# Kernel optimization log

Measured on AMD Instinct MI355X. Metric: run time of the kernel, lower is better.

The kernel has to match this reference:

```python
import jax, jax.numpy as jnp
import numpy as np

THRESHOLD = 0.7
STRIDE = 1
PADDING = 1


def setup_inputs() -> dict:
    key = jax.random.key(0)
    k1, k2 = jax.random.split(key)
    B, CIN, H, W = 32, 256, 56, 56
    COUT, K = 256, 3
    x = jax.random.normal(k1, (B, CIN, H, W), dtype=jnp.float32)
    # kaiming-uniform-ish init: U(-bound, bound), bound = sqrt(6/fan_in)
    fan_in = CIN * K * K
    bound = float(np.sqrt(6.0 / fan_in))
    weight = jax.random.uniform(k2, (COUT, CIN, K, K), dtype=jnp.float32,
                                minval=-bound, maxval=bound)
    alpha = jnp.ones((1,), dtype=jnp.float32)
    bias = jnp.zeros((COUT,), dtype=jnp.float32)
    return {"x": x, "weight": weight, "alpha": alpha, "bias": bias}


def _ternize_ste(w, threshold):
    delta = threshold * jnp.mean(jnp.abs(jax.lax.stop_gradient(w)))
    ternary = jnp.where(w > delta, 1.0,
                        jnp.where(w < -delta, -1.0, 0.0)).astype(w.dtype)
    # straight-through: value = ternary, gradient = identity w.r.t. w
    return ternary + (w - jax.lax.stop_gradient(w))


def reference(x, weight, alpha, bias):
    w_t = _ternize_ste(weight, THRESHOLD) * alpha  # [COUT, CIN, K, K]
    out = jax.lax.conv_general_dilated(
        x, w_t,
        window_strides=(STRIDE, STRIDE),
        padding=[(PADDING, PADDING), (PADDING, PADDING)],
        dimension_numbers=("NCHW", "OIHW", "NCHW"),
    )
    return out + bias[None, :, None, None]
```

## Files before the change

kernel.cpp:

```cpp
#include <hip/hip_runtime.h>

typedef unsigned short ushort_t;
typedef short short8 __attribute__((ext_vector_type(8)));
typedef unsigned short ushort8 __attribute__((ext_vector_type(8)));
typedef float floatx4 __attribute__((ext_vector_type(4)));

#define N_W 589824

static __device__ __forceinline__ unsigned short f2bf(float f) {
    unsigned int u = __float_as_uint(f);
    u = (u + 0x7FFFu + ((u >> 16) & 1u)) >> 16;
    return (unsigned short)u;
}

static __device__ __forceinline__ void g2l16(const void* g, void* lds_base_uniform) {
    __builtin_amdgcn_global_load_lds(
        (__attribute__((address_space(1))) void*)g,
        (__attribute__((address_space(3))) void*)lds_base_uniform,
        16, 0, 0);
}

__global__ void absmean_kernel(const float* __restrict__ w, double* __restrict__ dsum) {
    int tid = blockIdx.x * blockDim.x + threadIdx.x;
    int stride = gridDim.x * blockDim.x;
    float local = 0.f;
    for (int i = tid; i < N_W; i += stride) local += fabsf(w[i]);
    for (int off = 32; off > 0; off >>= 1)
        local += __shfl_down(local, off, 64);
    __shared__ float part[4];
    int lane = threadIdx.x & 63, wv = threadIdx.x >> 6;
    if (lane == 0) part[wv] = local;
    __syncthreads();
    if (threadIdx.x == 0) {
        float s = part[0] + part[1] + part[2] + part[3];
        atomicAdd(dsum, (double)s);
    }
}

__global__ void ternarize_frag_kernel(const float* __restrict__ w, const double* __restrict__ dsum,
                                      ushort_t* __restrict__ wtf) {
    int o = blockIdx.x * 256 + threadIdx.x;
    float delta = 0.7f * (float)(*dsum / (double)N_W);
    int e   = o & 7;
    int l   = (o >> 3) & 15;
    int q   = (o >> 7) & 3;
    int i   = (o >> 9) & 3;
    int g   = (o >> 11) & 3;
    int t13 = o >> 13;
    int r9  = t13 % 9;
    int cb  = t13 / 9;
    int co  = g * 64 + i * 16 + l;
    int cin = cb * 32 + q * 8 + e;
    float v = w[(co * 256 + cin) * 9 + r9];
    float t = (v > delta) ? 1.f : ((v < -delta) ? -1.f : 0.f);
    wtf[o] = f2bf(t);
}

__global__ void ternarize_kernel(const float* __restrict__ w, const double* __restrict__ dsum,
                                 ushort_t* __restrict__ wt) {
    int o = blockIdx.x * 256 + threadIdx.x;
    float delta = 0.7f * (float)(*dsum / (double)N_W);
    int cin = o & 255;
    int co  = (o >> 8) & 255;
    int r   = o >> 16;
    float v = w[(co * 256 + cin) * 9 + r];
    float t = (v > delta) ? 1.f : ((v < -delta) ? -1.f : 0.f);
    wt[o] = f2bf(t);
}

__global__ void border_zero_kernel(ushort_t* __restrict__ xp) {
    int e = blockIdx.x * 256 + threadIdx.x;
    int cg   = e & 31;
    int rest = e >> 5;
    int pid  = rest % 228;
    int b    = rest / 228;
    int hh, ww;
    if (pid < 58)       { hh = 0;  ww = pid; }
    else if (pid < 116) { hh = 57; ww = pid - 58; }
    else {
        int p = pid - 116;
        hh = 1 + (p >> 1);
        ww = (p & 1) ? 57 : 0;
    }
    ushort8 z = (ushort8){0,0,0,0,0,0,0,0};
    *(ushort8*)&xp[(((b * 58 + hh) * 58 + ww) << 8) + cg * 8] = z;
}

__global__ __launch_bounds__(256)
void xcvt_kernel(const float* __restrict__ x, ushort_t* __restrict__ xp) {
    __shared__ float tile[64][65];
    const int px0 = blockIdx.x * 64;
    const int ci0 = blockIdx.y * 64;
    const int b   = blockIdx.z;
    const int row  = threadIdx.x >> 6;
    const int lane = threadIdx.x & 63;
#pragma unroll
    for (int k = 0; k < 16; ++k) {
        int ci_l = row * 16 + k;
        tile[ci_l][lane] = x[(b * 256 + ci0 + ci_l) * 3136 + px0 + lane];
    }
    __syncthreads();
#pragma unroll
    for (int p = 0; p < 2; ++p) {
        int c    = threadIdx.x + p * 256;
        int px_l = c >> 3;
        int cg   = c & 7;
        int px = px0 + px_l;
        int h = px / 56, w = px - h * 56;
        ushort8 v;
#pragma unroll
        for (int j = 0; j < 8; ++j) v[j] = f2bf(tile[cg * 8 + j][px_l]);
        *(ushort8*)&xp[(((b * 58 + h + 1) * 58 + (w + 1)) << 8) + ci0 + cg * 8] = v;
    }
}

__global__ __launch_bounds__(256, 3)
void conv_mfma3_kernel(const ushort_t* __restrict__ xp, const ushort_t* __restrict__ wtf,
                       const float* __restrict__ alpha, const float* __restrict__ bias,
                       float* __restrict__ out) {
    __shared__ __align__(16) ushort_t lds_x[2 * 768 * 8];

    const int tid  = threadIdx.x;
    const int b    = blockIdx.y;
    const int th   = blockIdx.x >> 2;
    const int tw   = blockIdx.x & 3;
    const int h0   = th * 8;
    const int w0   = tw * 16;
    const int co0  = blockIdx.z * 128;

    const int lane = tid & 63;
    const int wave = tid >> 6;
    const int l15  = lane & 15;
    const int quad = lane >> 4;
    const int wco  = (wave & 1) * 64;
    const int wrow = (wave >> 1) * 4;

    unsigned goff[3], loff[3];
#pragma unroll
    for (int t = 0; t < 3; ++t) {
        int s = tid + t * 256;
        int ss = (s < 720) ? s : 719;
        int hr = ss / 72;
        int rem = ss - hr * 72;
        int hc = rem >> 2, cig = rem & 3;
        int gh = h0 + hr;
        int gw = w0 + hc; if (gw > 57) gw = 57;
        goff[t] = (unsigned)(((((b * 58 + gh) * 58 + gw) << 8) + (cig << 3)) * 2);
        loff[t] = (unsigned)((s & ~63) * 16);
    }
    const char* xpb = (const char*)xp;

    floatx4 acc[4][4];
#pragma unroll
    for (int i = 0; i < 4; ++i)
#pragma unroll
        for (int j = 0; j < 4; ++j)
            acc[i][j] = (floatx4){0.f, 0.f, 0.f, 0.f};

    const int gsel = blockIdx.z * 2 + (wave & 1);
    const ushort_t* wbase = wtf + gsel * 2048 + lane * 8;

#pragma unroll
    for (int t = 0; t < 3; ++t)
        g2l16(xpb + goff[t], (char*)lds_x + loff[t]);

    int cur = 0;
    for (int cb = 0; cb < 8; ++cb) {
        const ushort_t* wcb = wbase + cb * (9 * 4 * 2048);
        short8 af[3][4];
#pragma unroll
        for (int r = 0; r < 3; ++r)
#pragma unroll
            for (int i = 0; i < 4; ++i)
                af[r][i] = *(const short8*)(wcb + r * 8192 + i * 512);

        __syncthreads();

        if (cb < 7) {
#pragma unroll
            for (int t = 0; t < 3; ++t)
                g2l16(xpb + goff[t] + (cb + 1) * 64, (char*)lds_x + loff[t] + (cur ^ 1) * 12288);
        }

        const ushort_t* xb = lds_x + cur * 6144;

        short8 bfv[2][4];
#pragma unroll
        for (int j = 0; j < 4; ++j)
            bfv[0][j] = *(const short8*)&xb[((wrow + j + 0) * 18 + (l15 + 0)) * 32 + quad * 8];

#pragma unroll
        for (int r9 = 0; r9 < 9; ++r9) {
            if (r9 < 8) {
                const int kh1 = (r9 + 1) / 3;
                const int kw1 = (r9 + 1) - kh1 * 3;
#pragma unroll
                for (int j = 0; j < 4; ++j)
                    bfv[(r9 + 1) & 1][j] = *(const short8*)&xb[((wrow + j + kh1) * 18 + (l15 + kw1)) * 32 + quad * 8];
            }
#pragma unroll
            for (int i = 0; i < 4; ++i)
#pragma unroll
                for (int j = 0; j < 4; ++j)
                    acc[i][j] = __builtin_amdgcn_mfma_f32_16x16x32_bf16(af[r9 % 3][i], bfv[r9 & 1][j], acc[i][j], 0, 0, 0);
            if (r9 < 6) {
#pragma unroll
                for (int i = 0; i < 4; ++i)
                    af[r9 % 3][i] = *(const short8*)(wcb + (r9 + 3) * 8192 + i * 512);
            }
        }
        cur ^= 1;
    }

    const float a0 = alpha[0];
#pragma unroll
    for (int i = 0; i < 4; ++i) {
        int cob = co0 + wco + i * 16 + quad * 4;
#pragma unroll
        for (int j = 0; j < 4; ++j) {
            int hh = h0 + wrow + j;
            int ww = w0 + l15;
            if (ww < 56) {
#pragma unroll
                for (int r = 0; r < 4; ++r) {
                    int cog = cob + r;
                    out[((b * 256 + cog) * 56 + hh) * 56 + ww] = acc[i][j][r] * a0 + bias[cog];
                }
            }
        }
    }
}

__global__ __launch_bounds__(256, 2)
void conv_mfma_fallback_kernel(const float* __restrict__ x, const ushort_t* __restrict__ wt,
                               const float* __restrict__ alpha, const float* __restrict__ bias,
                               float* __restrict__ out) {
    __shared__ __align__(16) ushort_t lds_x[10 * 18 * 40];
    __shared__ __align__(16) ushort_t lds_a[128 * 40];
    const int tid  = threadIdx.x;
    const int b    = blockIdx.y;
    const int th   = blockIdx.x >> 2;
    const int tw   = blockIdx.x & 3;
    const int h0   = th * 8;
    const int w0   = tw * 16;
    const int co0  = blockIdx.z * 128;
    const int lane = tid & 63;
    const int wave = tid >> 6;
    const int l15  = lane & 15;
    const int quad = lane >> 4;
    const int wco  = (wave & 1) * 64;
    const int wrow = (wave >> 1) * 4;
    floatx4 acc[4][4];
#pragma unroll
    for (int i = 0; i < 4; ++i)
#pragma unroll
        for (int j = 0; j < 4; ++j)
            acc[i][j] = (floatx4){0.f, 0.f, 0.f, 0.f};
    const int co_l = tid >> 1;
    const int half = tid & 1;
    for (int cin0 = 0; cin0 < 256; cin0 += 32) {
        for (int e = tid; e < 5760; e += 256) {
            int hc = e % 18;
            int t2 = e / 18;
            int hr = t2 % 10;
            int ci = t2 / 10;
            int hh = h0 - 1 + hr;
            int ww = w0 - 1 + hc;
            float v = 0.f;
            if (hh >= 0 && hh < 56 && ww >= 0 && ww < 56)
                v = x[((b * 256 + cin0 + ci) * 3136) + hh * 56 + ww];
            lds_x[(hr * 18 + hc) * 40 + ci] = f2bf(v);
        }
        for (int r9 = 0; r9 < 9; ++r9) {
            {
                const short8* src = (const short8*)(wt + (((r9 * 256) + co0 + co_l) * 256 + cin0 + half * 16));
                short8 v0 = src[0];
                short8 v1 = src[1];
                *(short8*)&lds_a[co_l * 40 + half * 16]     = v0;
                *(short8*)&lds_a[co_l * 40 + half * 16 + 8] = v1;
            }
            __syncthreads();
            const int kh = r9 / 3;
            const int kw = r9 % 3;
            short8 af[4], bf[4];
#pragma unroll
            for (int j = 0; j < 4; ++j)
                bf[j] = *(const short8*)&lds_x[((wrow + j + kh) * 18 + (l15 + kw)) * 40 + quad * 8];
#pragma unroll
            for (int i = 0; i < 4; ++i)
                af[i] = *(const short8*)&lds_a[(wco + i * 16 + l15) * 40 + quad * 8];
#pragma unroll
            for (int i = 0; i < 4; ++i)
#pragma unroll
                for (int j = 0; j < 4; ++j)
                    acc[i][j] = __builtin_amdgcn_mfma_f32_16x16x32_bf16(af[i], bf[j], acc[i][j], 0, 0, 0);
            __syncthreads();
        }
    }
    const float a0 = alpha[0];
#pragma unroll
    for (int i = 0; i < 4; ++i) {
        int cob = co0 + wco + i * 16 + quad * 4;
#pragma unroll
        for (int j = 0; j < 4; ++j) {
            int hh = h0 + wrow + j;
            int ww = w0 + l15;
            if (ww < 56) {
#pragma unroll
                for (int r = 0; r < 4; ++r) {
                    int cog = cob + r;
                    out[((b * 256 + cog) * 56 + hh) * 56 + ww] = acc[i][j][r] * a0 + bias[cog];
                }
            }
        }
    }
}

extern "C" void kernel_launch(void* const* d_in, const int* in_sizes, int n_in,
                              void* d_out, int out_size, void* d_ws, size_t ws_size,
                              hipStream_t stream) {
    const float* x      = (const float*)d_in[0];
    const float* weight = (const float*)d_in[1];
    const float* alpha  = (const float*)d_in[2];
    const float* bias   = (const float*)d_in[3];
    float* out = (float*)d_out;

    double*   dsum = (double*)d_ws;
    ushort_t* wtf  = (ushort_t*)((char*)d_ws + 256);
    ushort_t* xp   = (ushort_t*)((char*)d_ws + 256 + 1179648);
    const size_t NEED = 256 + 1179648 + 55115776;

    hipMemsetAsync(d_ws, 0, 16, stream);
    absmean_kernel<<<256, 256, 0, stream>>>(weight, dsum);

    dim3 grid(28, 32, 2);
    if (ws_size >= NEED) {
        ternarize_frag_kernel<<<N_W / 256, 256, 0, stream>>>(weight, dsum, wtf);
        border_zero_kernel<<<912, 256, 0, stream>>>(xp);
        dim3 cgrid(49, 4, 32);
        xcvt_kernel<<<cgrid, 256, 0, stream>>>(x, xp);
        conv_mfma3_kernel<<<grid, 256, 0, stream>>>(xp, wtf, alpha, bias, out);
    } else {
        ternarize_kernel<<<N_W / 256, 256, 0, stream>>>(weight, dsum, wtf);
        conv_mfma_fallback_kernel<<<grid, 256, 0, stream>>>(x, wtf, alpha, bias, out);
    }
}
```

Measured before the change: 366.7 us.

## Retile conv to 8x8 pixels by all 256 output channels per block

The main conv kernel now gives each block an 8x8 pixel tile and all 256 output channels, with each wave owning 64 channels. Before, a block covered 8x16 pixels (with masked padding columns) and 128 channels. The aim is to drop the wasted padded columns, reuse each input halo across every output channel, and shrink the LDS footprint. Weight fragments for the next channel block are prefetched during the last taps, and s_setprio raises priority around the MFMA bursts. The cost is that each block now loads more weight data relative to the smaller activation tile, and the halo overhead grows.

```diff
diff --git a/kernel.cpp b/kernel.cpp
--- a/kernel.cpp
+++ b/kernel.cpp
@@ -115,36 +115,35 @@
 }
 
 __global__ __launch_bounds__(256, 3)
-void conv_mfma3_kernel(const ushort_t* __restrict__ xp, const ushort_t* __restrict__ wtf,
+void conv_mfma4_kernel(const ushort_t* __restrict__ xp, const ushort_t* __restrict__ wtf,
                        const float* __restrict__ alpha, const float* __restrict__ bias,
                        float* __restrict__ out) {
-    __shared__ __align__(16) ushort_t lds_x[2 * 768 * 8];
+    __shared__ __align__(16) ushort_t lds_x[2 * 512 * 8];
 
     const int tid  = threadIdx.x;
     const int b    = blockIdx.y;
-    const int th   = blockIdx.x >> 2;
-    const int tw   = blockIdx.x & 3;
+    const int th   = blockIdx.x / 7;
+    const int tw   = blockIdx.x - th * 7;
     const int h0   = th * 8;
-    const int w0   = tw * 16;
-    const int co0  = blockIdx.z * 128;
+    const int w0   = tw * 8;
 
     const int lane = tid & 63;
     const int wave = tid >> 6;
     const int l15  = lane & 15;
     const int quad = lane >> 4;
-    const int wco  = (wave & 1) * 64;
-    const int wrow = (wave >> 1) * 4;
-
-    unsigned goff[3], loff[3];
-#pragma unroll
-    for (int t = 0; t < 3; ++t) {
-        int s = tid + t * 256;
-        int ss = (s < 720) ? s : 719;
-        int hr = ss / 72;
-        int rem = ss - hr * 72;
-        int hc = rem >> 2, cig = rem & 3;
+    const int hs   = l15 >> 3;
+    const int ws   = l15 & 7;
+
+    unsigned goff[2], loff[2];
+#pragma unroll
+    for (int t = 0; t < 2; ++t) {
+        int s  = tid + t * 256;
+        int ss = (s < 400) ? s : 399;
+        int hr  = ss / 40;
+        int rem = ss - hr * 40;
+        int wc  = rem >> 2, cig = rem & 3;
         int gh = h0 + hr;
-        int gw = w0 + hc; if (gw > 57) gw = 57;
+        int gw = w0 + wc;
         goff[t] = (unsigned)(((((b * 58 + gh) * 58 + gw) << 8) + (cig << 3)) * 2);
         loff[t] = (unsigned)((s & ~63) * 16);
     }
@@ -157,37 +156,41 @@
         for (int j = 0; j < 4; ++j)
             acc[i][j] = (floatx4){0.f, 0.f, 0.f, 0.f};
 
-    const int gsel = blockIdx.z * 2 + (wave & 1);
+    const int gsel = wave;
     const ushort_t* wbase = wtf + gsel * 2048 + lane * 8;
 
-#pragma unroll
-    for (int t = 0; t < 3; ++t)
+    short8 af[3][4];
+#pragma unroll
+    for (int r = 0; r < 3; ++r)
+#pragma unroll
+        for (int i = 0; i < 4; ++i)
+            af[r][i] = *(const short8*)(wbase + r * 8192 + i * 512);
+
+#pragma unroll
+    for (int t = 0; t < 2; ++t)
         g2l16(xpb + goff[t], (char*)lds_x + loff[t]);
+
+    const int baseB = (hs * 10 + ws) * 32 + quad * 8;
 
     int cur = 0;
     for (int cb = 0; cb < 8; ++cb) {
-        const ushort_t* wcb = wbase + cb * (9 * 4 * 2048);
-        short8 af[3][4];
-#pragma unroll
-        for (int r = 0; r < 3; ++r)
-#pragma unroll
-            for (int i = 0; i < 4; ++i)
-                af[r][i] = *(const short8*)(wcb + r * 8192 + i * 512);
+        const ushort_t* wcb = wbase + cb * 73728;
+        const ushort_t* wnx = wbase + ((cb < 7) ? cb + 1 : cb) * 73728;
 
         __syncthreads();
 
         if (cb < 7) {
 #pragma unroll
-            for (int t = 0; t < 3; ++t)
-                g2l16(xpb + goff[t] + (cb + 1) * 64, (char*)lds_x + loff[t] + (cur ^ 1) * 12288);
-        }
-
-        const ushort_t* xb = lds_x + cur * 6144;
+            for (int t = 0; t < 2; ++t)
+                g2l16(xpb + goff[t] + (cb + 1) * 64, (char*)lds_x + loff[t] + (cur ^ 1) * 8192);
+        }
+
+        const ushort_t* xb = lds_x + cur * 4096;
 
         short8 bfv[2][4];
 #pragma unroll
         for (int j = 0; j < 4; ++j)
-            bfv[0][j] = *(const short8*)&xb[((wrow + j + 0) * 18 + (l15 + 0)) * 32 + quad * 8];
+            bfv[0][j] = *(const short8*)&xb[baseB + (j * 2) * 320];
 
 #pragma unroll
         for (int r9 = 0; r9 < 9; ++r9) {
@@ -196,17 +199,23 @@
                 const int kw1 = (r9 + 1) - kh1 * 3;
 #pragma unroll
                 for (int j = 0; j < 4; ++j)
-                    bfv[(r9 + 1) & 1][j] = *(const short8*)&xb[((wrow + j + kh1) * 18 + (l15 + kw1)) * 32 + quad * 8];
-            }
+                    bfv[(r9 + 1) & 1][j] =
+                        *(const short8*)&xb[baseB + ((j * 2 + kh1) * 10 + kw1) * 32];
+            }
+            __builtin_amdgcn_s_setprio(1);
 #pragma unroll
             for (int i = 0; i < 4; ++i)
 #pragma unroll
                 for (int j = 0; j < 4; ++j)
-                    acc[i][j] = __builtin_amdgcn_mfma_f32_16x16x32_bf16(af[r9 % 3][i], bfv[r9 & 1][j], acc[i][j], 0, 0, 0);
-            if (r9 < 6) {
+                    acc[i][j] = __builtin_amdgcn_mfma_f32_16x16x32_bf16(
+                        af[r9 % 3][i], bfv[r9 & 1][j], acc[i][j], 0, 0, 0);
+            __builtin_amdgcn_s_setprio(0);
+            {
+                const ushort_t* asrc = (r9 < 6) ? (wcb + (r9 + 3) * 8192)
+                                                : (wnx + (r9 - 6) * 8192);
 #pragma unroll
                 for (int i = 0; i < 4; ++i)
-                    af[r9 % 3][i] = *(const short8*)(wcb + (r9 + 3) * 8192 + i * 512);
+                    af[r9 % 3][i] = *(const short8*)(asrc + i * 512);
             }
         }
         cur ^= 1;
@@ -215,17 +224,15 @@
     const float a0 = alpha[0];
 #pragma unroll
     for (int i = 0; i < 4; ++i) {
-        int cob = co0 + wco + i * 16 + quad * 4;
+        int cob = gsel * 64 + i * 16 + quad * 4;
 #pragma unroll
         for (int j = 0; j < 4; ++j) {
-            int hh = h0 + wrow + j;
-            int ww = w0 + l15;
-            if (ww < 56) {
-#pragma unroll
-                for (int r = 0; r < 4; ++r) {
-                    int cog = cob + r;
-                    out[((b * 256 + cog) * 56 + hh) * 56 + ww] = acc[i][j][r] * a0 + bias[cog];
-                }
+            int hh = h0 + j * 2 + hs;
+            int ww = w0 + ws;
+#pragma unroll
+            for (int r = 0; r < 4; ++r) {
+                int cog = cob + r;
+                out[((b * 256 + cog) * 56 + hh) * 56 + ww] = acc[i][j][r] * a0 + bias[cog];
             }
         }
     }
@@ -333,15 +340,16 @@
     hipMemsetAsync(d_ws, 0, 16, stream);
     absmean_kernel<<<256, 256, 0, stream>>>(weight, dsum);
 
-    dim3 grid(28, 32, 2);
     if (ws_size >= NEED) {
         ternarize_frag_kernel<<<N_W / 256, 256, 0, stream>>>(weight, dsum, wtf);
         border_zero_kernel<<<912, 256, 0, stream>>>(xp);
         dim3 cgrid(49, 4, 32);
         xcvt_kernel<<<cgrid, 256, 0, stream>>>(x, xp);
-        conv_mfma3_kernel<<<grid, 256, 0, stream>>>(xp, wtf, alpha, bias, out);
+        dim3 grid(49, 32);
+        conv_mfma4_kernel<<<grid, 256, 0, stream>>>(xp, wtf, alpha, bias, out);
     } else {
         ternarize_kernel<<<N_W / 256, 256, 0, stream>>>(weight, dsum, wtf);
+        dim3 grid(28, 32, 2);
         conv_mfma_fallback_kernel<<<grid, 256, 0, stream>>>(x, wtf, alpha, bias, out);
     }
 }
```

Result: faster. 337.7 us (-7.9%).
